# Kernel optimization log

Measured on AMD Instinct MI355X. Metric: run time of the kernel, lower is better.

Reference implementation:

```python
import jax, jax.numpy as jnp
import numpy as np

D_MODEL = 512
D_STATE = 128
D_CONV = 4
EXPAND = 2
HEADDIM = 64
NLAYERS = 2
D_INNER = EXPAND * D_MODEL          # 1024
NHEADS = D_INNER // HEADDIM         # 16
CONV_DIM = D_INNER + 2 * D_STATE    # 1280 (x, B, C share the depthwise conv)
D_IN_PROJ = 2 * D_INNER + 2 * D_STATE + NHEADS  # 2320 (z, xBC, dt)
VOCAB = 40
SEQ = 64
BATCH = 512
NUM_CLASSES = 2
FC_HID = 128
EPS = 1e-5


def setup_inputs() -> dict:
    key = jax.random.key(0)
    ks = jax.random.split(key, 12)
    x = jax.random.randint(ks[0], (BATCH, SEQ), 0, VOCAB)
    emb = jax.random.uniform(ks[1], (VOCAB, D_MODEL), minval=-0.1, maxval=0.1)
    emb = emb.at[0].set(0.0)  # padding_idx=0
    pos = jax.random.normal(ks[2], (1, SEQ, D_MODEL)) * 0.02
    in_proj_w = jax.random.normal(ks[3], (NLAYERS, D_IN_PROJ, D_MODEL)) * 0.02
    conv_w = jax.random.normal(ks[4], (NLAYERS, CONV_DIM, D_CONV)) * 0.1
    conv_b = jnp.zeros((NLAYERS, CONV_DIM))
    dt0 = jax.random.uniform(ks[5], (NLAYERS, NHEADS), minval=1e-3, maxval=0.1)
    dt_bias = dt0 + jnp.log(-jnp.expm1(-dt0))  # inverse softplus of dt0
    A_log = jnp.log(jax.random.uniform(ks[6], (NLAYERS, NHEADS), minval=1.0, maxval=16.0))
    D_skip = jnp.ones((NLAYERS, NHEADS))
    norm_w = jnp.ones((NLAYERS, D_INNER))
    out_proj_w = jax.random.normal(ks[7], (NLAYERS, D_MODEL, D_INNER)) * 0.02
    ln_g = jnp.ones((NLAYERS, D_MODEL))
    ln_b = jnp.zeros((NLAYERS, D_MODEL))
    fc1_w = jax.random.uniform(ks[8], (FC_HID, D_MODEL), minval=-0.1, maxval=0.1)
    fc1_b = jnp.zeros((FC_HID,))
    fc2_w = jax.random.uniform(ks[9], (NUM_CLASSES, FC_HID), minval=-0.1, maxval=0.1)
    fc2_b = jnp.zeros((NUM_CLASSES,))
    return dict(x=x, emb=emb, pos=pos, in_proj_w=in_proj_w, conv_w=conv_w,
                conv_b=conv_b, dt_bias=dt_bias, A_log=A_log, D_skip=D_skip,
                norm_w=norm_w, out_proj_w=out_proj_w, ln_g=ln_g, ln_b=ln_b,
                fc1_w=fc1_w, fc1_b=fc1_b, fc2_w=fc2_w, fc2_b=fc2_b)


def _layernorm(h, g, b):
    mu = jnp.mean(h, axis=-1, keepdims=True)
    var = jnp.mean(jnp.square(h - mu), axis=-1, keepdims=True)
    return (h - mu) * jax.lax.rsqrt(var + EPS) * g + b


def _mamba2_block(h, in_proj_w, conv_w, conv_b, dt_bias, A_log, D_skip, norm_w, out_proj_w):
    b, s, _ = h.shape
    zxbcdt = jnp.einsum('bsd,ed->bse', h, in_proj_w)  # [b,s,D_IN_PROJ]
    z = zxbcdt[..., :D_INNER]
    xBC = zxbcdt[..., D_INNER:D_INNER + CONV_DIM]
    dt_raw = zxbcdt[..., D_INNER + CONV_DIM:]          # [b,s,NHEADS]
    # causal depthwise 1D conv + silu
    xBC_t = jnp.pad(jnp.swapaxes(xBC, 1, 2), ((0, 0), (0, 0), (D_CONV - 1, 0)))
    conv = jax.lax.conv_general_dilated(xBC_t, conv_w[:, None, :], (1,), 'VALID',
                                        feature_group_count=CONV_DIM)
    xBC = jax.nn.silu(jnp.swapaxes(conv + conv_b[None, :, None], 1, 2))
    xs = xBC[..., :D_INNER].reshape(b, s, NHEADS, HEADDIM)
    Bm = xBC[..., D_INNER:D_INNER + D_STATE]           # [b,s,n] (ngroups=1)
    Cm = xBC[..., D_INNER + D_STATE:]                  # [b,s,n]
    dt = jax.nn.softplus(dt_raw + dt_bias)             # [b,s,h]
    A = -jnp.exp(A_log)                                # [h], negative
    # exact quadratic (1-semiseparable) SSD form, equal to the selective scan
    cum = jnp.cumsum(dt * A, axis=1)                   # [b,s,h]
    diff = cum[:, :, None, :] - cum[:, None, :, :]     # [b,i,j,h] <= 0 for i>=j
    causal = jnp.tril(jnp.ones((s, s), dtype=bool))
    L = jnp.exp(jnp.where(causal[None, :, :, None], diff, -jnp.inf))  # decay mask
    scores = jnp.einsum('bin,bjn->bij', Cm, Bm)
    M = scores[..., None] * L                          # [b,i,j,h]
    y = jnp.einsum('bijh,bjh,bjhp->bihp', M, dt, xs)
    y = y + D_skip[None, None, :, None] * xs
    y = y.reshape(b, s, D_INNER)
    # gated RMSNorm
    y = y * jax.nn.silu(z)
    y = y * jax.lax.rsqrt(jnp.mean(jnp.square(y), axis=-1, keepdims=True) + EPS) * norm_w
    return jnp.einsum('bsi,di->bsd', y, out_proj_w)


def reference(x, emb, pos, in_proj_w, conv_w, conv_b, dt_bias, A_log, D_skip,
              norm_w, out_proj_w, ln_g, ln_b, fc1_w, fc1_b, fc2_w, fc2_b):
    h = emb[x] + pos[:, :x.shape[1], :]  # dropout is identity in eval
    for l in range(NLAYERS):
        y = _mamba2_block(h, in_proj_w[l], conv_w[l], conv_b[l], dt_bias[l],
                          A_log[l], D_skip[l], norm_w[l], out_proj_w[l])
        h = h + _layernorm(y, ln_g[l], ln_b[l])
    pm = (jnp.sum(h, axis=-1) != 0).astype(h.dtype)[..., None]  # [b,s,1]
    pooled = jnp.sum(h * pm, axis=1) / jnp.clip(jnp.sum(pm, axis=1), 1.0, None)
    hid = jax.nn.relu(pooled @ fc1_w.T + fc1_b)
    return hid @ fc2_w.T + fc2_b
```

## Files before the change

kernel.cpp:

```cpp
#include <hip/hip_runtime.h>
#include <hip/hip_bf16.h>

#define D_MODEL   512
#define D_STATE   128
#define D_CONV    4
#define HEADDIM   64
#define NLAYERS   2
#define D_INNER   1024
#define NHEADS    16
#define CONV_DIM  1280
#define D_IN_PROJ 2320
#define NPAD      2432
#define SEQ       64
#define BATCH     512
#define NTOK      (BATCH*SEQ)
#define FC_HID    128
#define EPS       1e-5f
#define YPITCH    1032

using bf16 = __hip_bfloat16;
typedef __bf16 bf16x8 __attribute__((ext_vector_type(8)));
typedef float  f32x4  __attribute__((ext_vector_type(4)));

__device__ __forceinline__ float b2f(bf16 v)  { return __bfloat162float(v); }
__device__ __forceinline__ bf16  f2b(float v) { return __float2bfloat16(v); }
__device__ __forceinline__ float bflo(unsigned u){ return __builtin_bit_cast(float, u << 16); }
__device__ __forceinline__ float bfhi(unsigned u){ return __builtin_bit_cast(float, u & 0xffff0000u); }

__device__ __forceinline__ void gl_lds16(const void* g, void* l) {
    __builtin_amdgcn_global_load_lds((const __attribute__((address_space(1))) void*)g,
                                     (__attribute__((address_space(3))) void*)l, 16, 0, 0);
}

__global__ __launch_bounds__(256) void k_embed(const int* __restrict__ x,
        const float* __restrict__ emb, const float* __restrict__ pos,
        bf16* __restrict__ hb) {
    int idx = blockIdx.x*256 + threadIdx.x;
    int d   = (idx & 127) * 4;
    int tok = idx >> 7;
    int s   = tok & (SEQ-1);
    int v   = x[tok];
    float4 e4 = *(const float4*)(emb + (size_t)v*D_MODEL + d);
    float4 p4 = *(const float4*)(pos + (size_t)s*D_MODEL + d);
    bf16 o[4] = { f2b(e4.x+p4.x), f2b(e4.y+p4.y), f2b(e4.z+p4.z), f2b(e4.w+p4.w) };
    *(uint2*)(hb + (size_t)tok*D_MODEL + d) = *(uint2*)&o[0];
}

__global__ __launch_bounds__(256) void k_cvtw(const float* __restrict__ src,
        bf16* __restrict__ dst, int R, int Kc, int total8) {
    int idx = blockIdx.x*256 + threadIdx.x;
    if (idx >= total8) return;
    int e0 = idx*8;
    int r = e0 / Kc, c = e0 % Kc;
    bf16 tb[8];
    if (r < R) {
        float4 f0 = *(const float4*)(src + (size_t)r*Kc + c);
        float4 f1 = *(const float4*)(src + (size_t)r*Kc + c + 4);
        tb[0]=f2b(f0.x); tb[1]=f2b(f0.y); tb[2]=f2b(f0.z); tb[3]=f2b(f0.w);
        tb[4]=f2b(f1.x); tb[5]=f2b(f1.y); tb[6]=f2b(f1.z); tb[7]=f2b(f1.w);
    } else {
        #pragma unroll
        for (int e=0;e<8;e++) tb[e] = f2b(0.f);
    }
    *(uint4*)(dst + (size_t)r*Kc + c) = *(uint4*)&tb[0];
}

template<int FUSE, int KDIM>
__global__ __launch_bounds__(256) void k_gemm128(const bf16* __restrict__ A,
        const bf16* __restrict__ B, bf16* __restrict__ C,
        bf16* __restrict__ xbcc, float* __restrict__ dt, float* __restrict__ cum,
        const float* __restrict__ cw, const float* __restrict__ cb,
        const float* __restrict__ dt_bias, const float* __restrict__ A_log,
        int Nout, int nbx, int ctok)
{
    constexpr int NT = KDIM / 64;
    __shared__ __align__(16) char lds[65536];
    bf16* Cs = (bf16*)lds;

    const int nwg = gridDim.x;
    const int q = nwg >> 3, r = nwg & 7;
    const int xcd = blockIdx.x & 7, loc = blockIdx.x >> 3;
    const int wg = ((xcd < r) ? xcd*(q+1) : r*(q+1) + (xcd-r)*q) + loc;
    const int m0 = (wg / nbx) * 128;
    const int n0 = (wg % nbx) * 128;

    const int t = threadIdx.x;
    const int wid = t >> 6, lane = t & 63;
    const int lr = lane & 15, lg = lane >> 4;
    const int wm = (wid >> 1)*64, wn = (wid & 1)*64;
    const int srow = wid*32;
    const int sr   = lane >> 3;
    const int scol = ((lane & 7) ^ sr) * 8;

    const bf16* Abase = A + (size_t)(m0 + srow + sr)*KDIM + scol;
    const bf16* Bbase = B + (size_t)(n0 + srow + sr)*KDIM + scol;

    f32x4 acc[4][4] = {};
    char* bc = lds;
    char* bn = lds + 32768;

    auto STAGE = [&](char* buf, int kk) {
        #pragma unroll
        for (int c = 0; c < 4; c++) {
            gl_lds16(Abase + (size_t)(c*8)*KDIM + kk, buf + (srow + c*8)*128);
            gl_lds16(Bbase + (size_t)(c*8)*KDIM + kk, buf + 16384 + (srow + c*8)*128);
        }
    };

    STAGE(bc, 0);
    asm volatile("s_waitcnt vmcnt(0)" ::: "memory");
    __builtin_amdgcn_s_barrier();

    #pragma unroll
    for (int kt = 0; kt < NT; kt++) {
        if (kt + 1 < NT) STAGE(bn, (kt+1)*64);
        #pragma unroll
        for (int ks = 0; ks < 64; ks += 32) {
            bf16x8 a[4], b[4];
            #pragma unroll
            for (int mi=0;mi<4;mi++) {
                int ra = wm + mi*16 + lr;
                a[mi] = *(const bf16x8*)(bc + ra*128 + ((((ks>>3)+lg) ^ (ra&7))<<4));
            }
            #pragma unroll
            for (int ni=0;ni<4;ni++) {
                int rb = wn + ni*16 + lr;
                b[ni] = *(const bf16x8*)(bc + 16384 + rb*128 + ((((ks>>3)+lg) ^ (rb&7))<<4));
            }
            __builtin_amdgcn_s_setprio(1);
            #pragma unroll
            for (int mi=0;mi<4;mi++)
                #pragma unroll
                for (int ni=0;ni<4;ni++)
                    acc[mi][ni] = __builtin_amdgcn_mfma_f32_16x16x32_bf16(a[mi], b[ni], acc[mi][ni], 0,0,0);
            __builtin_amdgcn_s_setprio(0);
        }
        asm volatile("s_waitcnt vmcnt(0)" ::: "memory");
        __builtin_amdgcn_s_barrier();
        char* tb2 = bc; bc = bn; bn = tb2;
    }
    __builtin_amdgcn_sched_barrier(0);

    #pragma unroll
    for (int mi=0;mi<4;mi++)
        #pragma unroll
        for (int ni=0;ni<4;ni++)
            #pragma unroll
            for (int rr=0;rr<4;rr++)
                Cs[(wm+mi*16+lg*4+rr)*136 + wn+ni*16+lr] = f2b(acc[mi][ni][rr]);
    __syncthreads();

    const int rsub = t >> 4;
    const int c8   = (t & 15) * 8;

    if (FUSE == 0 || n0 < 1024) {
        const int strd = (FUSE == 0) ? Nout : 1024;
        #pragma unroll
        for (int it = 0; it < 8; it++) {
            int row = it*16 + rsub;
            *(uint4*)(C + (size_t)(m0+row)*strd + n0 + c8) = *(const uint4*)&Cs[row*136 + c8];
        }
    } else if (n0 < 2304) {
        const int cbase = n0 - 1024 + c8;
        float4 wreg[8]; float bias[8];
        #pragma unroll
        for (int e=0;e<8;e++) wreg[e] = *(const float4*)(cw + (size_t)(cbase+e)*4);
        {
            float4 b0 = *(const float4*)(cb + cbase);
            float4 b1 = *(const float4*)(cb + cbase + 4);
            bias[0]=b0.x; bias[1]=b0.y; bias[2]=b0.z; bias[3]=b0.w;
            bias[4]=b1.x; bias[5]=b1.y; bias[6]=b1.z; bias[7]=b1.w;
        }
        #pragma unroll
        for (int it = 0; it < 8; it++) {
            int row = it*16 + rsub;
            int sl  = row & (SEQ-1);
            float m3 = (sl >= 3) ? 1.f : 0.f;
            float m2 = (sl >= 2) ? 1.f : 0.f;
            float m1 = (sl >= 1) ? 1.f : 0.f;
            const bf16* sm3 = &Cs[(row-3)*136 + c8];
            const bf16* sm2 = &Cs[(row-2)*136 + c8];
            const bf16* sm1 = &Cs[(row-1)*136 + c8];
            const bf16* sm0 = &Cs[(row  )*136 + c8];
            float a[8];
            #pragma unroll
            for (int e=0;e<8;e++) {
                a[e] = bias[e]
                     + m3 * b2f(sm3[e]) * wreg[e].x
                     + m2 * b2f(sm2[e]) * wreg[e].y
                     + m1 * b2f(sm1[e]) * wreg[e].z
                     +      b2f(sm0[e]) * wreg[e].w;
            }
            bf16 outv[8];
            #pragma unroll
            for (int e=0;e<8;e++) outv[e] = f2b(a[e] / (1.f + __expf(-a[e])));
            *(uint4*)(xbcc + (size_t)(m0+row)*CONV_DIM + cbase) = *(uint4*)&outv[0];
        }
    } else {
        for (int p = wid; p < 32; p += 4) {
            int sq = p >> 4, head = p & 15;
            float raw = b2f(Cs[(sq*64 + lane)*136 + head]) + dt_bias[head];
            float dval = (raw > 20.f) ? raw : log1pf(__expf(raw));
            float Ah = -__expf(A_log[head]);
            float cc = dval * Ah;
            #pragma unroll
            for (int o=1;o<64;o<<=1) { float v = __shfl_up(cc, o); if (lane >= o) cc += v; }
            int tok = m0 + sq*64 + lane;
            dt [(size_t)head*ctok + tok] = dval;
            cum[(size_t)head*ctok + tok] = cc;
        }
    }
}

__global__ __launch_bounds__(256) void k_ssd(const bf16* __restrict__ xbcc,
        const float* __restrict__ dt, const float* __restrict__ cum,
        const float* __restrict__ Dskip, bf16* zio,
        const float* __restrict__ nw, int ctok) {
    extern __shared__ __align__(16) char sm[];
    bf16* yb  = (bf16*)sm;
    bf16* Wb  = (bf16*)(sm + 64*YPITCH*2);
    bf16* xsT = (bf16*)(sm + 64*YPITCH*2 + 9216);
    const int b = blockIdx.x;
    const int t = threadIdx.x;
    const size_t tokbase = (size_t)b*SEQ;
    const int lane = t & 63, lr = lane & 15, lg = lane >> 4;
    const int w = t >> 6;
    const int i0 = w*16;

    f32x4 sacc[4] = {};
    {
        const bf16* Cbase = xbcc + tokbase*CONV_DIM + D_INNER + D_STATE;
        const bf16* Bbase = xbcc + tokbase*CONV_DIM + D_INNER;
        #pragma unroll
        for (int ks = 0; ks < D_STATE; ks += 32) {
            bf16x8 af = *(const bf16x8*)(Cbase + (size_t)(i0+lr)*CONV_DIM + ks + lg*8);
            #pragma unroll
            for (int jt = 0; jt < 4; jt++) {
                bf16x8 bfr = *(const bf16x8*)(Bbase + (size_t)(jt*16+lr)*CONV_DIM + ks + lg*8);
                sacc[jt] = __builtin_amdgcn_mfma_f32_16x16x32_bf16(af, bfr, sacc[jt], 0,0,0);
            }
        }
    }

    for (int hh = 0; hh < NHEADS; hh++) {
        const size_t cbase = (size_t)hh*ctok + tokbase;
        __syncthreads();

        #pragma unroll
        for (int cc = 0; cc < 2; cc++) {
            int ch = cc*256 + t;
            int rr = ch >> 3, c8 = (ch & 7)*8;
            uint4 v = *(const uint4*)(xbcc + (tokbase + rr)*CONV_DIM + hh*HEADDIM + c8);
            const bf16* pv = (const bf16*)&v;
            #pragma unroll
            for (int e=0;e<8;e++) xsT[(c8+e)*72 + rr] = pv[e];
        }
        {
            float cum_i[4], cum_j[4], dt_j[4];
            #pragma unroll
            for (int rr=0;rr<4;rr++) cum_i[rr] = cum[cbase + i0 + lg*4 + rr];
            #pragma unroll
            for (int jt=0;jt<4;jt++) { int j = jt*16+lr; cum_j[jt]=cum[cbase+j]; dt_j[jt]=dt[cbase+j]; }
            #pragma unroll
            for (int jt=0;jt<4;jt++)
                #pragma unroll
                for (int rr=0;rr<4;rr++) {
                    int i = i0 + lg*4 + rr, j = jt*16 + lr;
                    float wv = (j <= i) ? sacc[jt][rr] * __expf(cum_i[rr]-cum_j[jt]) * dt_j[jt] : 0.f;
                    Wb[i*72 + j] = f2b(wv);
                }
        }
        __syncthreads();

        {
            float dsk = Dskip[hh];
            f32x4 yacc[4] = {};
            #pragma unroll
            for (int ks = 0; ks < 64; ks += 32) {
                bf16x8 a = *(const bf16x8*)&Wb[(w*16 + lr)*72 + ks + lg*8];
                #pragma unroll
                for (int n=0; n<4; n++) {
                    bf16x8 bb = *(const bf16x8*)&xsT[(n*16 + lr)*72 + ks + lg*8];
                    yacc[n] = __builtin_amdgcn_mfma_f32_16x16x32_bf16(a, bb, yacc[n], 0,0,0);
                }
            }
            #pragma unroll
            for (int n=0; n<4; n++)
                #pragma unroll
                for (int rr=0; rr<4; rr++) {
                    int row = w*16 + lg*4 + rr;
                    int col = n*16 + lr;
                    yb[row*YPITCH + hh*HEADDIM + col] = f2b(yacc[n][rr] + dsk * b2f(xsT[col*72 + row]));
                }
        }
    }
    __syncthreads();

    for (int pass = 0; pass < 16; pass++) {
        const int tok = pass*4 + w;
        const int d0  = lane*16;
        bf16* zrow        = zio + (tokbase + tok)*D_INNER + d0;
        const bf16* ybrow = yb + tok*YPITCH + d0;
        uint4 yv0 = *(const uint4*)(ybrow);
        uint4 yv1 = *(const uint4*)(ybrow + 8);
        uint4 zv0 = *(const uint4*)(zrow);
        uint4 zv1 = *(const uint4*)(zrow + 8);
        const unsigned* yu0 = (const unsigned*)&yv0;
        const unsigned* yu1 = (const unsigned*)&yv1;
        const unsigned* zu0 = (const unsigned*)&zv0;
        const unsigned* zu1 = (const unsigned*)&zv1;
        float g[16]; float ss = 0.f;
        #pragma unroll
        for (int e=0;e<4;e++) {
            float y0 = bflo(yu0[e]), y1 = bfhi(yu0[e]);
            float z0 = bflo(zu0[e]), z1 = bfhi(zu0[e]);
            float g0 = y0 * z0 / (1.f + __expf(-z0));
            float g1 = y1 * z1 / (1.f + __expf(-z1));
            g[2*e] = g0; g[2*e+1] = g1;
            ss += g0*g0 + g1*g1;
            float y2 = bflo(yu1[e]), y3 = bfhi(yu1[e]);
            float z2 = bflo(zu1[e]), z3 = bfhi(zu1[e]);
            float g2 = y2 * z2 / (1.f + __expf(-z2));
            float g3 = y3 * z3 / (1.f + __expf(-z3));
            g[8+2*e] = g2; g[8+2*e+1] = g3;
            ss += g2*g2 + g3*g3;
        }
        #pragma unroll
        for (int o=32;o>0;o>>=1) ss += __shfl_xor(ss, o);
        float scale = rsqrtf(ss/(float)D_INNER + EPS);
        bf16 outv[16];
        #pragma unroll
        for (int e=0;e<16;e++) outv[e] = f2b(g[e] * scale * nw[d0+e]);
        *(uint4*)zrow     = *(uint4*)&outv[0];
        *(uint4*)(zrow+8) = *(uint4*)&outv[8];
    }
}

__global__ __launch_bounds__(256) void k_resln(bf16* __restrict__ hb,
        const bf16* __restrict__ tmp,
        const float* __restrict__ g, const float* __restrict__ bb) {
    const int w = threadIdx.x >> 6, lane = threadIdx.x & 63;
    const size_t tok = (size_t)blockIdx.x*4 + w;
    const int d = lane*8;
    const size_t base = tok*D_MODEL + d;
    uint4 u4 = *(const uint4*)(tmp + base);
    const unsigned* uu = (const unsigned*)&u4;
    float v[8];
    #pragma unroll
    for (int e=0;e<4;e++) { v[2*e]=bflo(uu[e]); v[2*e+1]=bfhi(uu[e]); }
    float s=0.f, q=0.f;
    #pragma unroll
    for (int e=0;e<8;e++){ s += v[e]; q += v[e]*v[e]; }
    #pragma unroll
    for (int o=32;o>0;o>>=1){ s += __shfl_xor(s,o); q += __shfl_xor(q,o); }
    float mu  = s/(float)D_MODEL;
    float var = q/(float)D_MODEL - mu*mu;
    float inv = rsqrtf(var + EPS);
    uint4 h4 = *(const uint4*)(hb + base);
    const unsigned* hu = (const unsigned*)&h4;
    float4 g0 = *(const float4*)(g + d);
    float4 g1 = *(const float4*)(g + d + 4);
    float4 b0 = *(const float4*)(bb + d);
    float4 b1 = *(const float4*)(bb + d + 4);
    const float* gp0 = (const float*)&g0; const float* gp1 = (const float*)&g1;
    const float* bp0 = (const float*)&b0; const float* bp1 = (const float*)&b1;
    bf16 o8[8];
    #pragma unroll
    for (int e=0;e<4;e++) {
        float ge0 = (2*e < 4)   ? gp0[2*e]   : gp1[2*e-4];
        float ge1 = (2*e+1 < 4) ? gp0[2*e+1] : gp1[2*e+1-4];
        float be0 = (2*e < 4)   ? bp0[2*e]   : bp1[2*e-4];
        float be1 = (2*e+1 < 4) ? bp0[2*e+1] : bp1[2*e+1-4];
        float h0 = bflo(hu[e]) + (v[2*e]  -mu)*inv*ge0 + be0;
        float h1 = bfhi(hu[e]) + (v[2*e+1]-mu)*inv*ge1 + be1;
        o8[2*e] = f2b(h0); o8[2*e+1] = f2b(h1);
    }
    *(uint4*)(hb + base) = *(uint4*)&o8[0];
}

__global__ __launch_bounds__(256) void k_pool(const bf16* __restrict__ hb,
        float* __restrict__ pooled) {
    int b = blockIdx.x, t = threadIdx.x;
    __shared__ float ps[64][4];
    __shared__ float pm[64];
    __shared__ float cntS;
    {
        int s = t >> 2, qq = t & 3;
        const bf16* row = hb + ((size_t)b*SEQ + s)*D_MODEL + qq*128;
        float acc = 0;
        #pragma unroll
        for (int e=0;e<16;e++) {
            uint4 v = *(const uint4*)(row + e*8);
            const unsigned* vu = (const unsigned*)&v;
            #pragma unroll
            for (int k=0;k<4;k++) acc += bflo(vu[k]) + bfhi(vu[k]);
        }
        ps[s][qq] = acc;
    }
    __syncthreads();
    if (t < 64) pm[t] = (ps[t][0]+ps[t][1]+ps[t][2]+ps[t][3]) != 0.f ? 1.f : 0.f;
    __syncthreads();
    if (t == 0) { float c=0; for (int s2=0;s2<64;s2++) c+=pm[s2]; cntS = fmaxf(c,1.f); }
    __syncthreads();
    float cnt = cntS;
    #pragma unroll
    for (int rep=0;rep<2;rep++) {
        int d = t + rep*256;
        float acc = 0;
        for (int s2=0;s2<64;s2++)
            acc += b2f(hb[((size_t)b*SEQ+s2)*D_MODEL + d]) * pm[s2];
        pooled[(size_t)b*D_MODEL + d] = acc / cnt;
    }
}

__global__ __launch_bounds__(128) void k_fc(const float* __restrict__ pooled,
        const float* __restrict__ w1, const float* __restrict__ b1,
        const float* __restrict__ w2, const float* __restrict__ b2,
        float* __restrict__ out) {
    int b = blockIdx.x, j = threadIdx.x;
    __shared__ float hid[FC_HID];
    const float* p  = pooled + (size_t)b*D_MODEL;
    const float* wr = w1 + (size_t)j*D_MODEL;
    float acc = b1[j];
    for (int d=0; d<D_MODEL; d+=4)
        acc += p[d]*wr[d] + p[d+1]*wr[d+1] + p[d+2]*wr[d+2] + p[d+3]*wr[d+3];
    hid[j] = fmaxf(acc, 0.f);
    __syncthreads();
    if (j < 2) {
        float o = b2[j];
        for (int k=0;k<FC_HID;k++) o += hid[k]*w2[j*FC_HID+k];
        out[b*2 + j] = o;
    }
}

extern "C" void kernel_launch(void* const* d_in, const int* in_sizes, int n_in,
                              void* d_out, int out_size, void* d_ws, size_t ws_size,
                              hipStream_t stream) {
    (void)in_sizes; (void)n_in; (void)out_size;
    const int*   x        = (const int*)  d_in[0];
    const float* emb      = (const float*)d_in[1];
    const float* pos      = (const float*)d_in[2];
    const float* in_proj  = (const float*)d_in[3];
    const float* conv_w   = (const float*)d_in[4];
    const float* conv_b   = (const float*)d_in[5];
    const float* dt_bias  = (const float*)d_in[6];
    const float* A_log    = (const float*)d_in[7];
    const float* D_skip   = (const float*)d_in[8];
    const float* norm_w   = (const float*)d_in[9];
    const float* out_proj = (const float*)d_in[10];
    const float* ln_g     = (const float*)d_in[11];
    const float* ln_b     = (const float*)d_in[12];
    const float* fc1_w    = (const float*)d_in[13];
    const float* fc1_b    = (const float*)d_in[14];
    const float* fc2_w    = (const float*)d_in[15];
    const float* fc2_b    = (const float*)d_in[16];
    float* out = (float*)d_out;

    const int SSD_LDS = 64*YPITCH*2 + 2*9216;
    (void)hipFuncSetAttribute((const void*)k_ssd,
            hipFuncAttributeMaxDynamicSharedMemorySize, SSD_LDS);

    const size_t HB_B  = (size_t)NTOK * D_MODEL * 2;
    const size_t WPI_B = (size_t)NPAD * D_MODEL * 2;
    const size_t WPO_B = (size_t)D_MODEL * D_INNER * 2;
    const size_t PBASE = HB_B + NLAYERS*(WPI_B + WPO_B);

    const size_t PER_TOK = 2048 + 2560 + 128;
    int CB = BATCH;
    while (CB > 8 && PBASE + (size_t)CB*SEQ*PER_TOK > ws_size) CB >>= 1;
    const int CT = CB * SEQ;
    const int NC = BATCH / CB;

    char* ws = (char*)d_ws;
    bf16*  hb   = (bf16*) (ws);
    bf16*  wpi  = (bf16*) (ws + HB_B);
    bf16*  wpo  = (bf16*) (ws + HB_B + NLAYERS*WPI_B);
    char*  tr   = ws + PBASE;
    bf16*  zbuf = (bf16*) (tr);
    bf16*  xbcc = (bf16*) (tr + (size_t)CT*2048);
    float* dt   = (float*)(tr + (size_t)CT*(2048+2560));
    float* cum  = dt + (size_t)CT*NHEADS;
    bf16*  tmp  = xbcc;
    float* pooled = (float*)tr;

    for (int l = 0; l < NLAYERS; l++) {
        int t8i = NPAD*D_MODEL/8;
        k_cvtw<<<(t8i+255)/256, 256, 0, stream>>>(in_proj + (size_t)l*D_IN_PROJ*D_MODEL,
                wpi + (size_t)l*NPAD*D_MODEL, D_IN_PROJ, D_MODEL, t8i);
        int t8o = D_MODEL*D_INNER/8;
        k_cvtw<<<(t8o+255)/256, 256, 0, stream>>>(out_proj + (size_t)l*D_MODEL*D_INNER,
                wpo + (size_t)l*D_MODEL*D_INNER, D_MODEL, D_INNER, t8o);
    }

    k_embed<<<(NTOK*128)/256, 256, 0, stream>>>(x, emb, pos, hb);

    const int NBX_I = NPAD/128;
    const int NBX_O = D_MODEL/128;

    for (int l = 0; l < NLAYERS; l++) {
        const bf16* wi = wpi + (size_t)l*NPAD*D_MODEL;
        const bf16* wo = wpo + (size_t)l*D_MODEL*D_INNER;
        for (int c = 0; c < NC; c++) {
            const int tok0 = c * CT;
            bf16* hbc = hb + (size_t)tok0 * D_MODEL;
            k_gemm128<1,512><<<(CT/128)*NBX_I, 256, 0, stream>>>(hbc, wi, zbuf,
                    xbcc, dt, cum,
                    conv_w + (size_t)l*CONV_DIM*D_CONV, conv_b + (size_t)l*CONV_DIM,
                    dt_bias + l*NHEADS, A_log + l*NHEADS,
                    NPAD, NBX_I, CT);
            k_ssd<<<CB, 256, SSD_LDS, stream>>>(xbcc, dt, cum, D_skip + l*NHEADS,
                    zbuf, norm_w + (size_t)l*D_INNER, CT);
            k_gemm128<0,1024><<<(CT/128)*NBX_O, 256, 0, stream>>>(zbuf, wo, tmp,
                    nullptr, nullptr, nullptr, nullptr, nullptr, nullptr, nullptr,
                    D_MODEL, NBX_O, CT);
            k_resln<<<CT/4, 256, 0, stream>>>(hbc, tmp, ln_g + l*D_MODEL, ln_b + l*D_MODEL);
        }
    }

    k_pool<<<BATCH, 256, 0, stream>>>(hb, pooled);
    k_fc<<<BATCH, FC_HID, 0, stream>>>(pooled, fc1_w, fc1_b, fc2_w, fc2_b, out);
}
```

Baseline: 589.0 us.

## Split SSD kernel into two row-half blocks per sequence

Each sequence is now handled by two blocks, each computing 32 output rows, which doubles the grid and roughly halves the LDS per block. The aim is higher occupancy and better CU utilization for the SSD stage. In exchange, each block still loads the full xs/B/cum data, so that work is duplicated. Only half the waves compute scores and decay weights, leaving the other two waves idle in that phase.

```diff
diff --git a/kernel.cpp b/kernel.cpp
--- a/kernel.cpp
+++ b/kernel.cpp
@@ -218,17 +218,20 @@
         const float* __restrict__ nw, int ctok) {
     extern __shared__ __align__(16) char sm[];
     bf16* yb  = (bf16*)sm;
-    bf16* Wb  = (bf16*)(sm + 64*YPITCH*2);
-    bf16* xsT = (bf16*)(sm + 64*YPITCH*2 + 9216);
-    const int b = blockIdx.x;
+    bf16* Wb  = (bf16*)(sm + 32*YPITCH*2);
+    bf16* xsT = (bf16*)(sm + 32*YPITCH*2 + 4608);
+    const int bid = blockIdx.x;
+    const int b   = bid >> 1;
+    const int r0  = (bid & 1) * 32;
     const int t = threadIdx.x;
     const size_t tokbase = (size_t)b*SEQ;
     const int lane = t & 63, lr = lane & 15, lg = lane >> 4;
     const int w = t >> 6;
-    const int i0 = w*16;
 
     f32x4 sacc[4] = {};
-    {
+    const int irel0 = (w & 1) * 16;
+    if (w < 2) {
+        const int i0 = r0 + irel0;
         const bf16* Cbase = xbcc + tokbase*CONV_DIM + D_INNER + D_STATE;
         const bf16* Bbase = xbcc + tokbase*CONV_DIM + D_INNER;
         #pragma unroll
@@ -255,52 +258,55 @@
             #pragma unroll
             for (int e=0;e<8;e++) xsT[(c8+e)*72 + rr] = pv[e];
         }
-        {
+        if (w < 2) {
             float cum_i[4], cum_j[4], dt_j[4];
             #pragma unroll
-            for (int rr=0;rr<4;rr++) cum_i[rr] = cum[cbase + i0 + lg*4 + rr];
+            for (int rr=0;rr<4;rr++) cum_i[rr] = cum[cbase + r0 + irel0 + lg*4 + rr];
             #pragma unroll
             for (int jt=0;jt<4;jt++) { int j = jt*16+lr; cum_j[jt]=cum[cbase+j]; dt_j[jt]=dt[cbase+j]; }
             #pragma unroll
             for (int jt=0;jt<4;jt++)
                 #pragma unroll
                 for (int rr=0;rr<4;rr++) {
-                    int i = i0 + lg*4 + rr, j = jt*16 + lr;
-                    float wv = (j <= i) ? sacc[jt][rr] * __expf(cum_i[rr]-cum_j[jt]) * dt_j[jt] : 0.f;
-                    Wb[i*72 + j] = f2b(wv);
+                    int irel = irel0 + lg*4 + rr, j = jt*16 + lr;
+                    float wv = (j <= r0 + irel)
+                             ? sacc[jt][rr] * __expf(cum_i[rr]-cum_j[jt]) * dt_j[jt] : 0.f;
+                    Wb[irel*72 + j] = f2b(wv);
                 }
         }
         __syncthreads();
 
         {
             float dsk = Dskip[hh];
-            f32x4 yacc[4] = {};
+            const int ro = (w & 1) * 16, co = (w >> 1) * 32;
+            f32x4 yacc[2] = {};
             #pragma unroll
             for (int ks = 0; ks < 64; ks += 32) {
-                bf16x8 a = *(const bf16x8*)&Wb[(w*16 + lr)*72 + ks + lg*8];
+                bf16x8 a = *(const bf16x8*)&Wb[(ro + lr)*72 + ks + lg*8];
                 #pragma unroll
-                for (int n=0; n<4; n++) {
-                    bf16x8 bb = *(const bf16x8*)&xsT[(n*16 + lr)*72 + ks + lg*8];
+                for (int n=0; n<2; n++) {
+                    bf16x8 bb = *(const bf16x8*)&xsT[(co + n*16 + lr)*72 + ks + lg*8];
                     yacc[n] = __builtin_amdgcn_mfma_f32_16x16x32_bf16(a, bb, yacc[n], 0,0,0);
                 }
             }
             #pragma unroll
-            for (int n=0; n<4; n++)
+            for (int n=0; n<2; n++)
                 #pragma unroll
                 for (int rr=0; rr<4; rr++) {
-                    int row = w*16 + lg*4 + rr;
-                    int col = n*16 + lr;
-                    yb[row*YPITCH + hh*HEADDIM + col] = f2b(yacc[n][rr] + dsk * b2f(xsT[col*72 + row]));
+                    int row = ro + lg*4 + rr;
+                    int col = co + n*16 + lr;
+                    yb[row*YPITCH + hh*HEADDIM + col] =
+                        f2b(yacc[n][rr] + dsk * b2f(xsT[col*72 + (r0 + row)]));
                 }
         }
     }
     __syncthreads();
 
-    for (int pass = 0; pass < 16; pass++) {
-        const int tok = pass*4 + w;
+    for (int pass = 0; pass < 8; pass++) {
+        const int trel = pass*4 + w;
         const int d0  = lane*16;
-        bf16* zrow        = zio + (tokbase + tok)*D_INNER + d0;
-        const bf16* ybrow = yb + tok*YPITCH + d0;
+        bf16* zrow        = zio + (tokbase + r0 + trel)*D_INNER + d0;
+        const bf16* ybrow = yb + trel*YPITCH + d0;
         uint4 yv0 = *(const uint4*)(ybrow);
         uint4 yv1 = *(const uint4*)(ybrow + 8);
         uint4 zv0 = *(const uint4*)(zrow);
@@ -456,7 +462,7 @@
     const float* fc2_b    = (const float*)d_in[16];
     float* out = (float*)d_out;
 
-    const int SSD_LDS = 64*YPITCH*2 + 2*9216;
+    const int SSD_LDS = 32*YPITCH*2 + 4608 + 9216;
     (void)hipFuncSetAttribute((const void*)k_ssd,
             hipFuncAttributeMaxDynamicSharedMemorySize, SSD_LDS);
 
@@ -508,7 +514,7 @@
                     conv_w + (size_t)l*CONV_DIM*D_CONV, conv_b + (size_t)l*CONV_DIM,
                     dt_bias + l*NHEADS, A_log + l*NHEADS,
                     NPAD, NBX_I, CT);
-            k_ssd<<<CB, 256, SSD_LDS, stream>>>(xbcc, dt, cum, D_skip + l*NHEADS,
+            k_ssd<<<CB*2, 256, SSD_LDS, stream>>>(xbcc, dt, cum, D_skip + l*NHEADS,
                     zbuf, norm_w + (size_t)l*D_INNER, CT);
             k_gemm128<0,1024><<<(CT/128)*NBX_O, 256, 0, stream>>>(zbuf, wo, tmp,
                     nullptr, nullptr, nullptr, nullptr, nullptr, nullptr, nullptr,
```

New measurement: 583.7 us. Within noise of the previous version (-0.9%).
